# Kernel optimization log

Hardware: AMD Instinct MI355X
Metric: run time of the kernel (lower is better)

## Reference

```python
import jax, jax.numpy as jnp
import numpy as np

B, D_IN, D_OUT, E = 8192, 1024, 1024, 16

def setup_inputs() -> dict:
    key = jax.random.key(0)
    k1, k2, k3 = jax.random.split(key, 3)
    scale_in = 1.0 / np.sqrt(D_IN)
    return {
        "x": jax.random.normal(k1, (B, D_IN), dtype=jnp.float32),
        "Wg": jax.random.normal(k2, (D_IN, E), dtype=jnp.float32) * scale_in,
        "bg": jnp.zeros((E,), dtype=jnp.float32),
        "We": jax.random.normal(k3, (E, D_IN, D_OUT), dtype=jnp.float32) * scale_in,
        "be": jnp.zeros((E, D_OUT), dtype=jnp.float32),
    }

def reference(x, Wg, bg, We, be):
    # gate: Linear + softmax over experts  -> [B, E]
    gate_probs = jax.nn.softmax(x @ Wg + bg, axis=1)
    # all experts as one batched GEMM: [B, E, D_OUT]
    expert_outputs = jnp.einsum("bi,eio->beo", x, We) + be[None, :, :]
    # gate-weighted sum over experts -> [B, D_OUT]
    return jnp.einsum("be,beo->bo", gate_probs, expert_outputs)
```

## Files before the change

### kernel.cpp

```cpp
#include <hip/hip_runtime.h>
#include <hip/hip_bf16.h>

#define NB 8192
#define DIN 1024
#define DOUT 1024
#define NE 16

#define BM 256
#define BN 256
#define BK 32
#define NT 256

typedef __attribute__((ext_vector_type(8))) short bf16x8;
typedef __attribute__((ext_vector_type(4))) short short4_t;
typedef __attribute__((ext_vector_type(4))) float f32x4;

__device__ __forceinline__ unsigned short f32_to_bf16(float f) {
  unsigned int u = __float_as_uint(f);
  u += 0x7FFFu + ((u >> 16) & 1u);
  return (unsigned short)(u >> 16);
}

__device__ __forceinline__ void gl_lds16(const void* gp, void* lp) {
  __builtin_amdgcn_global_load_lds(
      (const __attribute__((address_space(1))) void*)gp,
      (__attribute__((address_space(3))) void*)lp, 16, 0, 0);
}

#define SB __builtin_amdgcn_sched_barrier(0)

__global__ __launch_bounds__(256) void gate_cast_kernel(
    const float* __restrict__ x, const float* __restrict__ Wg,
    const float* __restrict__ bg, float* __restrict__ gout,
    unsigned short* __restrict__ xbf) {
  const int lane = threadIdx.x & 63;
  const int wid = threadIdx.x >> 6;
  const int row = blockIdx.x * 4 + wid;

  const f32x4* xr = (const f32x4*)(x + (size_t)row * DIN);
  f32x4 xv[4];
#pragma unroll
  for (int j = 0; j < 4; ++j) xv[j] = xr[j * 64 + lane];

  float acc[NE];
#pragma unroll
  for (int e = 0; e < NE; ++e) acc[e] = 0.f;

#pragma unroll
  for (int j = 0; j < 4; ++j) {
#pragma unroll
    for (int t = 0; t < 4; ++t) {
      const int i = j * 256 + lane * 4 + t;
      const f32x4* wrow = (const f32x4*)(Wg + (size_t)i * NE);
      const f32x4 w0 = wrow[0], w1 = wrow[1], w2 = wrow[2], w3 = wrow[3];
      const float xx = xv[j][t];
#pragma unroll
      for (int q = 0; q < 4; ++q) {
        acc[q]      = fmaf(xx, w0[q], acc[q]);
        acc[4 + q]  = fmaf(xx, w1[q], acc[4 + q]);
        acc[8 + q]  = fmaf(xx, w2[q], acc[8 + q]);
        acc[12 + q] = fmaf(xx, w3[q], acc[12 + q]);
      }
    }
  }
#pragma unroll
  for (int off = 32; off >= 1; off >>= 1) {
#pragma unroll
    for (int e = 0; e < NE; ++e) acc[e] += __shfl_xor(acc[e], off, 64);
  }
#pragma unroll
  for (int e = 0; e < NE; ++e) acc[e] += bg[e];
  float mx = acc[0];
#pragma unroll
  for (int e = 1; e < NE; ++e) mx = fmaxf(mx, acc[e]);
  float p[NE];
  float s = 0.f;
#pragma unroll
  for (int e = 0; e < NE; ++e) { p[e] = expf(acc[e] - mx); s += p[e]; }
  const float inv = 1.f / s;
  if (lane == 0) {
#pragma unroll
    for (int e = 0; e < NE; ++e) gout[(size_t)row * NE + e] = p[e] * inv;
  }
#pragma unroll
  for (int j = 0; j < 4; ++j) {
    short4_t o;
#pragma unroll
    for (int t = 0; t < 4; ++t) o[t] = (short)f32_to_bf16(xv[j][t]);
    *(short4_t*)(xbf + (size_t)row * DIN + j * 256 + lane * 4) = o;
  }
}

__global__ __launch_bounds__(256) void we_transpose_kernel(
    const float* __restrict__ We, unsigned short* __restrict__ WeT) {
  __shared__ float tile[64][65];
  const int e = blockIdx.z, it = blockIdx.y, ot = blockIdx.x;
  const int tr = threadIdx.x >> 4;
  const int tc = (threadIdx.x & 15) * 4;
  const float* src = We + (((size_t)e * DIN + it * 64) * DOUT) + ot * 64;
#pragma unroll
  for (int rr = 0; rr < 64; rr += 16) {
    const f32x4 v = *(const f32x4*)(src + (size_t)(rr + tr) * DOUT + tc);
#pragma unroll
    for (int t = 0; t < 4; ++t) tile[rr + tr][tc + t] = v[t];
  }
  __syncthreads();
  unsigned short* dst = WeT + (((size_t)e * DOUT + ot * 64) * DIN) + it * 64;
#pragma unroll
  for (int rr = 0; rr < 64; rr += 16) {
    short4_t o;
#pragma unroll
    for (int t = 0; t < 4; ++t) o[t] = (short)f32_to_bf16(tile[tc + t][rr + tr]);
    *(short4_t*)(dst + (size_t)(rr + tr) * DIN + tc) = o;
  }
}

__global__ __launch_bounds__(512, 2) void moe_gemm_kernel(
    const unsigned short* __restrict__ xbf,
    const unsigned short* __restrict__ WeT,
    const float* __restrict__ g,
    const float* __restrict__ be,
    float* __restrict__ out) {
  __shared__ __align__(16) unsigned short As[4][BM * BK];
  __shared__ __align__(16) unsigned short Bs[4][BN * BK];
  __shared__ float gs[BM][NE];

  const int tid = threadIdx.x;
  const int lane = tid & 63, wid = tid >> 6;
  const int wm = wid >> 2, wn = wid & 3;
  const int l15 = lane & 15, l4 = lane >> 4;

  const int bid = blockIdx.x;
  const int xcd = bid & 7, jj_ = bid >> 3;
  const int kh = xcd >> 2;
  const int brow = ((xcd & 3) * 8 + (jj_ >> 2)) * BM;
  const int bcol = (jj_ & 3) * BN;

  const int rswz = ((l4 ^ (l15 & 3)) << 4);
  const char* const ldsA = (const char*)&As[0][0] + (wm * 128 + l15) * 64 + rswz;
  const char* const ldsB = (const char*)&Bs[0][0] + (wn * 64 + l15) * 64 + rswz;

  const int srow = tid >> 2;
  const int lk = ((((tid & 3) << 4) ^ ((srow & 3) << 4)) >> 1);
  const unsigned short* const aBase = xbf + (size_t)(brow + srow) * DIN + lk;
  const unsigned short* const bBase = WeT + (size_t)(bcol + srow) * DIN + lk;
  char* const ldsStA = (char*)&As[0][0] + wid * 1024;
  char* const ldsStB = (char*)&Bs[0][0] + wid * 1024;

#define STA(BUF, CR, KC) \
  gl_lds16(aBase + (size_t)(CR) * DIN + (KC), ldsStA + (BUF) * 16384 + (CR) * 64)
#define STB(BUF, CR, EOFF, KC) \
  gl_lds16(bBase + (EOFF) + (size_t)(CR) * DIN + (KC), \
           ldsStB + (BUF) * 16384 + (CR) * 64)
#define RD_B(BUF)                                                  \
  _Pragma("unroll") for (int ni = 0; ni < 4; ++ni)                 \
      bfr[ni] = *(const bf16x8*)(ldsB + ni * 1024 + (BUF) * 16384);
#define RD_A(MI0, BUF)                                             \
  _Pragma("unroll") for (int d = 0; d < 4; ++d)                    \
      af[d] = *(const bf16x8*)(ldsA + ((MI0) + d) * 1024 + (BUF) * 16384);
#define MFMA_P(MI0)                                                \
  _Pragma("unroll") for (int d = 0; d < 4; ++d)                    \
  _Pragma("unroll") for (int ni = 0; ni < 4; ++ni)                 \
      acc[(MI0) + d][ni] = __builtin_amdgcn_mfma_f32_16x16x32_bf16(\
          af[d], bfr[ni], acc[(MI0) + d][ni], 0, 0, 0);

  {
    const f32x4* gsrc = (const f32x4*)(g + (size_t)brow * NE);
    f32x4* gdst = (f32x4*)&gs[0][0];
    gdst[tid] = gsrc[tid];
    gdst[tid + 512] = gsrc[tid + 512];
  }

  {
    const size_t e0 = (size_t)(kh * 8) * (size_t)(DIN * DOUT);
    STB(0, 0, e0, 0);  STB(0, 128, e0, 0);  STA(0, 0, 0);  STA(0, 128, 0);
    STB(1, 0, e0, 32); STB(1, 128, e0, 32); STA(1, 0, 32); STA(1, 128, 32);
    STB(2, 0, e0, 64); STB(2, 128, e0, 64); STA(2, 0, 64); STA(2, 128, 64);
  }

  f32x4 acc[8][4];
#pragma unroll
  for (int mi = 0; mi < 8; ++mi)
#pragma unroll
    for (int ni = 0; ni < 4; ++ni) acc[mi][ni] = (f32x4){0.f, 0.f, 0.f, 0.f};

  asm volatile("s_waitcnt vmcnt(8) lgkmcnt(0)" ::: "memory");
  __builtin_amdgcn_s_barrier(); SB;

  bf16x8 bfr[4], af[4];

#define TILE_BODY(T, BUF)                                                      \
  {                                                                            \
    const int t_ = (T);                                                        \
    const int sT = t_ + 3;                                                     \
    const bool doStage = sT < NT;                                              \
    const int bufS = ((BUF) + 3) & 3;                                          \
    const int kcS = (sT & 31) * 32;                                            \
    const size_t eoffS =                                                       \
        (size_t)(kh * 8 + (sT >> 5)) * (size_t)(DIN * DOUT);                   \
    if ((t_ & 31) == 0 && t_ > 0) {               \
      const int e = kh * 8 + (t_ >> 5);                                        \
      _Pragma("unroll") for (int mi = 0; mi < 8; ++mi) {                       \
        const int rb = wm * 128 + mi * 16 + l4 * 4;                            \
        _Pragma("unroll") for (int q = 0; q < 4; ++q) {                        \
          const float r = gs[rb + q][e - 1] *                                  \
                          __builtin_amdgcn_rcpf(fmaxf(gs[rb + q][e], 1e-30f)); \
          _Pragma("unroll") for (int ni = 0; ni < 4; ++ni)                     \
              acc[mi][ni][q] *= r;                                             \
        }                                                                      \
      }                                                                        \
    }                                                                          \
                                                    \
    RD_B(BUF); RD_A(0, BUF);                                                   \
    if (doStage) { STB(bufS, 0, eoffS, kcS); STB(bufS, 128, eoffS, kcS); }     \
    __builtin_amdgcn_s_barrier(); SB;                                          \
    __builtin_amdgcn_s_setprio(1); MFMA_P(0);                                  \
    __builtin_amdgcn_s_setprio(0);                                             \
                                                    \
    RD_A(4, BUF);                                                              \
    if (doStage) { STA(bufS, 0, kcS); STA(bufS, 128, kcS); }                   \
    __builtin_amdgcn_s_barrier(); SB;                                          \
    __builtin_amdgcn_s_setprio(1); MFMA_P(4);                                  \
    __builtin_amdgcn_s_setprio(0);                                             \
    if ((t_ & 31) == 31) {                              \
      const int e = kh * 8 + (t_ >> 5);                                        \
      _Pragma("unroll") for (int ni = 0; ni < 4; ++ni) {                       \
        const float bv = be[e * DOUT + bcol + wn * 64 + ni * 16 + l15];        \
        _Pragma("unroll") for (int mi = 0; mi < 8; ++mi)                       \
          _Pragma("unroll") for (int q = 0; q < 4; ++q)                        \
              acc[mi][ni][q] += bv;                                            \
      }                                                                        \
    }                                                                          \
                            \
    if (t_ < NT - 3) { asm volatile("s_waitcnt vmcnt(8)" ::: "memory"); }      \
    else if (t_ == NT - 3) { asm volatile("s_waitcnt vmcnt(4)" ::: "memory"); }\
    else if (t_ == NT - 2) { asm volatile("s_waitcnt vmcnt(0)" ::: "memory"); }\
    if (t_ < NT - 1) { __builtin_amdgcn_s_barrier(); SB; }                     \
  }

  for (int tt = 0; tt < NT; tt += 4) {
    TILE_BODY(tt, 0);
    TILE_BODY(tt + 1, 1);
    TILE_BODY(tt + 2, 2);
    TILE_BODY(tt + 3, 3);
  }

  const int eL = kh * 8 + 7;
  float bv[8][4];
#pragma unroll
  for (int e8 = 0; e8 < 8; ++e8)
#pragma unroll
    for (int ni = 0; ni < 4; ++ni)
      bv[e8][ni] = be[(kh * 8 + e8) * DOUT + bcol + wn * 64 + ni * 16 + l15];
#pragma unroll
  for (int mi = 0; mi < 8; ++mi) {
    const int rb = wm * 128 + mi * 16 + l4 * 4;
#pragma unroll
    for (int q = 0; q < 4; ++q) {
      const int row = rb + q;
      const float gf = gs[row][eL];
      float b0 = 0.f, b1 = 0.f, b2 = 0.f, b3 = 0.f;
#pragma unroll
      for (int e8 = 0; e8 < 8; ++e8) {
        const float ge = gs[row][kh * 8 + e8];
        b0 = fmaf(ge, bv[e8][0], b0);
        b1 = fmaf(ge, bv[e8][1], b1);
        b2 = fmaf(ge, bv[e8][2], b2);
        b3 = fmaf(ge, bv[e8][3], b3);
      }
      float* const orp =
          out + (size_t)(brow + row) * DOUT + bcol + wn * 64 + l15;
      atomicAdd(orp,      fmaf(acc[mi][0][q], gf, b0));
      atomicAdd(orp + 16, fmaf(acc[mi][1][q], gf, b1));
      atomicAdd(orp + 32, fmaf(acc[mi][2][q], gf, b2));
      atomicAdd(orp + 48, fmaf(acc[mi][3][q], gf, b3));
    }
  }
#undef TILE_BODY
#undef MFMA_P
#undef RD_A
#undef RD_B
#undef STA
#undef STB
}

extern "C" void kernel_launch(void* const* d_in, const int* in_sizes, int n_in,
                              void* d_out, int out_size, void* d_ws, size_t ws_size,
                              hipStream_t stream) {
  const float* x  = (const float*)d_in[0];
  const float* Wg = (const float*)d_in[1];
  const float* bg = (const float*)d_in[2];
  const float* We = (const float*)d_in[3];
  const float* be = (const float*)d_in[4];
  float* out = (float*)d_out;

  char* ws = (char*)d_ws;
  unsigned short* xbf = (unsigned short*)ws;
  unsigned short* WeT = (unsigned short*)(ws + (size_t)NB * DIN * 2);
  float* g = (float*)(ws + (size_t)NB * DIN * 2 + (size_t)NE * DIN * DOUT * 2);

  hipMemsetAsync(out, 0, (size_t)NB * DOUT * sizeof(float), stream);
  gate_cast_kernel<<<dim3(NB / 4), 256, 0, stream>>>(x, Wg, bg, g, xbf);
  we_transpose_kernel<<<dim3(DOUT / 64, DIN / 64, NE), 256, 0, stream>>>(We, WeT);
  moe_gemm_kernel<<<dim3(256), 512, 0, stream>>>(xbf, WeT, g, be, out);
}
```

Measured before the change: 380.8 us.

## Restructure GEMM main loop into two-slab iterations with fewer barriers

Reworks the main loop so each iteration processes two K-slabs from the 4-buffer ring. Each slab is staged with a single grouped load of A and B, and the vmcnt waits move to the start of each slab, which removes the trailing per-tile barrier. It also changes the LDS swizzle pattern and loads only the 8 gate columns this block needs into a smaller shared array. The intent is to cut barrier and sync overhead and LDS bank conflicts, but the wait counts and buffer indexing are harder to get right.

Result: no change. 383.1 us (+0.6%).

```diff
diff --git a/kernel.cpp b/kernel.cpp
--- a/kernel.cpp
+++ b/kernel.cpp
@@ -8,8 +8,7 @@
 
 #define BM 256
 #define BN 256
-#define BK 32
-#define NT 256
+#define NT 128
 
 typedef __attribute__((ext_vector_type(8))) short bf16x8;
 typedef __attribute__((ext_vector_type(4))) short short4_t;
@@ -121,9 +120,9 @@
     const float* __restrict__ g,
     const float* __restrict__ be,
     float* __restrict__ out) {
-  __shared__ __align__(16) unsigned short As[4][BM * BK];
-  __shared__ __align__(16) unsigned short Bs[4][BN * BK];
-  __shared__ float gs[BM][NE];
+  __shared__ __align__(16) unsigned short As[4][BM * 32];
+  __shared__ __align__(16) unsigned short Bs[4][BN * 32];
+  __shared__ float gs[BM][8];
 
   const int tid = threadIdx.x;
   const int lane = tid & 63, wid = tid >> 6;
@@ -136,28 +135,34 @@
   const int brow = ((xcd & 3) * 8 + (jj_ >> 2)) * BM;
   const int bcol = (jj_ & 3) * BN;
 
-  const int rswz = ((l4 ^ (l15 & 3)) << 4);
-  const char* const ldsA = (const char*)&As[0][0] + (wm * 128 + l15) * 64 + rswz;
-  const char* const ldsB = (const char*)&Bs[0][0] + (wn * 64 + l15) * 64 + rswz;
+  const int swzr = (l4 ^ ((l15 >> 1) & 3)) << 4;
+  const int ldsAoff = (wm * 128 + l15) * 64 + swzr;
+  const int ldsBoff = (wn * 64 + l15) * 64 + swzr;
+  const char* const AsB = (const char*)&As[0][0];
+  const char* const BsB = (const char*)&Bs[0][0];
 
   const int srow = tid >> 2;
-  const int lk = ((((tid & 3) << 4) ^ ((srow & 3) << 4)) >> 1);
-  const unsigned short* const aBase = xbf + (size_t)(brow + srow) * DIN + lk;
-  const unsigned short* const bBase = WeT + (size_t)(bcol + srow) * DIN + lk;
-  char* const ldsStA = (char*)&As[0][0] + wid * 1024;
-  char* const ldsStB = (char*)&Bs[0][0] + wid * 1024;
-
-#define STA(BUF, CR, KC) \
-  gl_lds16(aBase + (size_t)(CR) * DIN + (KC), ldsStA + (BUF) * 16384 + (CR) * 64)
-#define STB(BUF, CR, EOFF, KC) \
-  gl_lds16(bBase + (EOFF) + (size_t)(CR) * DIN + (KC), \
-           ldsStB + (BUF) * 16384 + (CR) * 64)
-#define RD_B(BUF)                                                  \
-  _Pragma("unroll") for (int ni = 0; ni < 4; ++ni)                 \
-      bfr[ni] = *(const bf16x8*)(ldsB + ni * 1024 + (BUF) * 16384);
-#define RD_A(MI0, BUF)                                             \
-  _Pragma("unroll") for (int d = 0; d < 4; ++d)                    \
-      af[d] = *(const bf16x8*)(ldsA + ((MI0) + d) * 1024 + (BUF) * 16384);
+  const int lk = (((tid & 3) ^ ((srow >> 1) & 3)) << 3);
+  const unsigned short* const aB = xbf + (size_t)(brow + srow) * DIN + lk;
+  const unsigned short* const bB = WeT + (size_t)(bcol + srow) * DIN + lk;
+  char* const dstA = (char*)&As[0][0] + wid * 1024;
+  char* const dstB = (char*)&Bs[0][0] + wid * 1024;
+
+#define STSLAB(BUFI, S)                                                  \
+  {                                                                      \
+    const int kc_ = ((S) & 31) * 32;                                     \
+    const size_t eo_ = (size_t)(kh * 8 + ((S) >> 5)) * (size_t)(DIN * DOUT); \
+    gl_lds16(aB + kc_, dstA + (BUFI) * 16384);                           \
+    gl_lds16(aB + 131072 + kc_, dstA + (BUFI) * 16384 + 8192);           \
+    gl_lds16(bB + eo_ + kc_, dstB + (BUFI) * 16384);                     \
+    gl_lds16(bB + eo_ + 131072 + kc_, dstB + (BUFI) * 16384 + 8192);     \
+  }
+#define RD_B(BI)                                                  \
+  _Pragma("unroll") for (int ni = 0; ni < 4; ++ni)                \
+      bfr[ni] = *(const bf16x8*)(BsB + (BI) * 16384 + ldsBoff + ni * 1024);
+#define RD_A(MI0, BI)                                             \
+  _Pragma("unroll") for (int d = 0; d < 4; ++d)                   \
+      af[d] = *(const bf16x8*)(AsB + (BI) * 16384 + ldsAoff + ((MI0) + d) * 1024);
 #define MFMA_P(MI0)                                                \
   _Pragma("unroll") for (int d = 0; d < 4; ++d)                    \
   _Pragma("unroll") for (int ni = 0; ni < 4; ++ni)                 \
@@ -165,18 +170,15 @@
           af[d], bfr[ni], acc[(MI0) + d][ni], 0, 0, 0);
 
   {
-    const f32x4* gsrc = (const f32x4*)(g + (size_t)brow * NE);
-    f32x4* gdst = (f32x4*)&gs[0][0];
-    gdst[tid] = gsrc[tid];
-    gdst[tid + 512] = gsrc[tid + 512];
-  }
-
-  {
-    const size_t e0 = (size_t)(kh * 8) * (size_t)(DIN * DOUT);
-    STB(0, 0, e0, 0);  STB(0, 128, e0, 0);  STA(0, 0, 0);  STA(0, 128, 0);
-    STB(1, 0, e0, 32); STB(1, 128, e0, 32); STA(1, 0, 32); STA(1, 128, 32);
-    STB(2, 0, e0, 64); STB(2, 128, e0, 64); STA(2, 0, 64); STA(2, 128, 64);
-  }
+    const float* gsrc = g + (size_t)brow * NE + kh * 8;
+    const int grow = tid >> 1, gh = tid & 1;
+    const f32x4 v = *(const f32x4*)(gsrc + (size_t)grow * NE + gh * 4);
+    ((f32x4*)&gs[0][0])[tid] = v;
+  }
+
+  STSLAB(0, 0);
+  STSLAB(1, 1);
+  STSLAB(2, 2);
 
   f32x4 acc[8][4];
 #pragma unroll
@@ -184,46 +186,53 @@
 #pragma unroll
     for (int ni = 0; ni < 4; ++ni) acc[mi][ni] = (f32x4){0.f, 0.f, 0.f, 0.f};
 
-  asm volatile("s_waitcnt vmcnt(8) lgkmcnt(0)" ::: "memory");
-  __builtin_amdgcn_s_barrier(); SB;
-
   bf16x8 bfr[4], af[4];
 
-#define TILE_BODY(T, BUF)                                                      \
+#define TILE_BODY(T, B0, B1, S0B, S3B)                                         \
   {                                                                            \
     const int t_ = (T);                                                        \
-    const int sT = t_ + 3;                                                     \
-    const bool doStage = sT < NT;                                              \
-    const int bufS = ((BUF) + 3) & 3;                                          \
-    const int kcS = (sT & 31) * 32;                                            \
-    const size_t eoffS =                                                       \
-        (size_t)(kh * 8 + (sT >> 5)) * (size_t)(DIN * DOUT);                   \
-    if ((t_ & 31) == 0 && t_ > 0) {               \
-      const int e = kh * 8 + (t_ >> 5);                                        \
+    if ((t_ & 15) == 0 && t_ > 0) {               \
+      const int e8 = t_ >> 4;                                                  \
       _Pragma("unroll") for (int mi = 0; mi < 8; ++mi) {                       \
         const int rb = wm * 128 + mi * 16 + l4 * 4;                            \
         _Pragma("unroll") for (int q = 0; q < 4; ++q) {                        \
-          const float r = gs[rb + q][e - 1] *                                  \
-                          __builtin_amdgcn_rcpf(fmaxf(gs[rb + q][e], 1e-30f)); \
+          const float r = gs[rb + q][e8 - 1] *                                 \
+                          __builtin_amdgcn_rcpf(fmaxf(gs[rb + q][e8], 1e-30f));\
           _Pragma("unroll") for (int ni = 0; ni < 4; ++ni)                     \
               acc[mi][ni][q] *= r;                                             \
         }                                                                      \
       }                                                                        \
     }                                                                          \
-                                                    \
-    RD_B(BUF); RD_A(0, BUF);                                                   \
-    if (doStage) { STB(bufS, 0, eoffS, kcS); STB(bufS, 128, eoffS, kcS); }     \
+                                           \
+    if (t_ < NT - 1) { asm volatile("s_waitcnt vmcnt(8)" ::: "memory"); }      \
+    else             { asm volatile("s_waitcnt vmcnt(4)" ::: "memory"); }      \
+    SB;                                                                        \
+    RD_B(B0); RD_A(0, B0);                                                     \
+    if (t_ <= NT - 2) STSLAB(S0B, 2 * t_ + 3);                                 \
     __builtin_amdgcn_s_barrier(); SB;                                          \
     __builtin_amdgcn_s_setprio(1); MFMA_P(0);                                  \
     __builtin_amdgcn_s_setprio(0);                                             \
-                                                    \
-    RD_A(4, BUF);                                                              \
-    if (doStage) { STA(bufS, 0, kcS); STA(bufS, 128, kcS); }                   \
+                            \
+    RD_A(4, B0);                                                               \
     __builtin_amdgcn_s_barrier(); SB;                                          \
     __builtin_amdgcn_s_setprio(1); MFMA_P(4);                                  \
     __builtin_amdgcn_s_setprio(0);                                             \
-    if ((t_ & 31) == 31) {                              \
-      const int e = kh * 8 + (t_ >> 5);                                        \
+                                         \
+    if (t_ < NT - 1) { asm volatile("s_waitcnt vmcnt(8)" ::: "memory"); }      \
+    else             { asm volatile("s_waitcnt vmcnt(0)" ::: "memory"); }      \
+    SB;                                                                        \
+    RD_B(B1); RD_A(0, B1);                                                     \
+    __builtin_amdgcn_s_barrier(); SB;                                          \
+    __builtin_amdgcn_s_setprio(1); MFMA_P(0);                                  \
+    __builtin_amdgcn_s_setprio(0);                                             \
+                        \
+    RD_A(4, B1);                                                               \
+    if (t_ <= NT - 3) STSLAB(S3B, 2 * t_ + 4);                                 \
+    __builtin_amdgcn_s_barrier(); SB;                                          \
+    __builtin_amdgcn_s_setprio(1); MFMA_P(4);                                  \
+    __builtin_amdgcn_s_setprio(0);                                             \
+    if ((t_ & 15) == 15) {                             \
+      const int e = kh * 8 + (t_ >> 4);                                        \
       _Pragma("unroll") for (int ni = 0; ni < 4; ++ni) {                       \
         const float bv = be[e * DOUT + bcol + wn * 64 + ni * 16 + l15];        \
         _Pragma("unroll") for (int mi = 0; mi < 8; ++mi)                       \
@@ -231,21 +240,13 @@
               acc[mi][ni][q] += bv;                                            \
       }                                                                        \
     }                                                                          \
-                            \
-    if (t_ < NT - 3) { asm volatile("s_waitcnt vmcnt(8)" ::: "memory"); }      \
-    else if (t_ == NT - 3) { asm volatile("s_waitcnt vmcnt(4)" ::: "memory"); }\
-    else if (t_ == NT - 2) { asm volatile("s_waitcnt vmcnt(0)" ::: "memory"); }\
-    if (t_ < NT - 1) { __builtin_amdgcn_s_barrier(); SB; }                     \
-  }
-
-  for (int tt = 0; tt < NT; tt += 4) {
-    TILE_BODY(tt, 0);
-    TILE_BODY(tt + 1, 1);
-    TILE_BODY(tt + 2, 2);
-    TILE_BODY(tt + 3, 3);
-  }
-
-  const int eL = kh * 8 + 7;
+  }
+
+  for (int tt = 0; tt < NT; tt += 2) {
+    TILE_BODY(tt, 0, 1, 3, 0);
+    TILE_BODY(tt + 1, 2, 3, 1, 2);
+  }
+
   float bv[8][4];
 #pragma unroll
   for (int e8 = 0; e8 < 8; ++e8)
@@ -258,11 +259,11 @@
 #pragma unroll
     for (int q = 0; q < 4; ++q) {
       const int row = rb + q;
-      const float gf = gs[row][eL];
+      const float gf = gs[row][7];
       float b0 = 0.f, b1 = 0.f, b2 = 0.f, b3 = 0.f;
 #pragma unroll
       for (int e8 = 0; e8 < 8; ++e8) {
-        const float ge = gs[row][kh * 8 + e8];
+        const float ge = gs[row][e8];
         b0 = fmaf(ge, bv[e8][0], b0);
         b1 = fmaf(ge, bv[e8][1], b1);
         b2 = fmaf(ge, bv[e8][2], b2);
@@ -280,8 +281,7 @@
 #undef MFMA_P
 #undef RD_A
 #undef RD_B
-#undef STA
-#undef STB
+#undef STSLAB
 }
 
 extern "C" void kernel_launch(void* const* d_in, const int* in_sizes, int n_in,
```
